# Optimization experiments

Hardware: AMD Instinct MI355X
Metric: run time of the kernel (lower is better)

The kernel has to match this reference:

```python
import jax, jax.numpy as jnp
import numpy as np

B, T, M = 4, 1024, 512
H, K, V = 8, 64, 64
EPS = 1e-6


def setup_inputs() -> dict:
    key = jax.random.key(0)
    ks = jax.random.split(key, 8)
    s = 1.0 / np.sqrt(M)
    return {
        "query": jax.random.normal(ks[0], (B, T, M), jnp.float32),
        "key": jax.random.normal(ks[1], (B, T, M), jnp.float32),
        "value": jax.random.normal(ks[2], (B, T, M), jnp.float32),
        "Wq": jax.random.normal(ks[3], (M, H * K), jnp.float32) * s,
        "Wk": jax.random.normal(ks[4], (M, H * K), jnp.float32) * s,
        "Wv": jax.random.normal(ks[5], (M, H * V), jnp.float32) * s,
        # gate linear is zero-initialized in the original (Constant(0.0)); use
        # small random weights so the gate path is exercised numerically.
        "Wg": jax.random.normal(ks[6], (M, H * V), jnp.float32) * (0.02 * s),
        "bg": jnp.zeros((H * V,), jnp.float32),
        "Wo": jax.random.normal(ks[7], (H * V, M), jnp.float32) * (1.0 / np.sqrt(H * V)),
    }


def _phi(x):
    return jax.nn.elu(x) + 1.0


def reference(query, key, value, Wq, Wk, Wv, Wg, bg, Wo):
    # projections -> [B, T, H, d]
    q = (query @ Wq).reshape(B, T, H, K)
    k = (key @ Wk).reshape(B, T, H, K)
    v = (value @ Wv).reshape(B, T, H, V)

    qf = _phi(q)
    kf = _phi(k)

    # multiplicative value gate from the raw value input
    gate = jax.nn.sigmoid((value @ Wg + bg).reshape(B, T, H, V))
    v = v * (2.0 * gate)

    # visualization attention map: qf . kf, causal, row-normalized
    scores = jnp.einsum("bthk,bshk->bhts", qf, kf)  # [B,H,T,T]
    causal = (jnp.arange(T)[None, :] <= jnp.arange(T)[:, None]).astype(scores.dtype)
    scores = scores * causal[None, None]
    att_map = scores / (jnp.sum(scores, axis=-1, keepdims=True) + EPS)

    # causal linear attention via cumulative sums (Tq == Tk so the idx-take
    # in the original is an identity gather)
    kv = jnp.einsum("bthk,bthv->bthkv", kf, v)  # [B,T,H,K,V]
    kv_cum = jnp.cumsum(kv, axis=1)
    k_cum = jnp.cumsum(kf, axis=1)               # [B,T,H,K]

    numer = jnp.einsum("bthk,bthkv->bthv", qf, kv_cum)
    denom = jnp.einsum("bthk,bthk->bth", qf, k_cum) + EPS
    out = (numer / denom[..., None]).reshape(B, T, H * V)
    out = out @ Wo  # [B,T,M]
    return out, att_map
```

## Files before the change

### kernel.cpp

```cpp
#include <hip/hip_runtime.h>
#include <cstdint>

#define TDIM 1024
#define BDIM 4
#define EPSF 1e-6f

#define OFF_KSUM  32768u
#define OFF_KV    65536u
#define FLOAT_BYTES 8650752u
#define UOFF_QP 0u
#define UOFF_KP 2097152u
#define UOFF_VP 4194304u
#define UOFF_NB 6291456u
#define UOFF_WQ 8388608u
#define UOFF_WK 8650752u
#define UOFF_WV 8912896u
#define UOFF_WG 9175040u
#define UOFF_WO 9437184u

typedef short bf16x8 __attribute__((ext_vector_type(8)));
typedef float f32x4  __attribute__((ext_vector_type(4)));
typedef unsigned short ushort_t;

union bfu { int4 i4; unsigned short us[8]; bf16x8 v; };

__device__ __forceinline__ float phi_f(float x)  { return x > 0.f ? x + 1.f : __expf(x); }
__device__ __forceinline__ float sigm_f(float x) { return 1.f / (1.f + __expf(-x)); }
__device__ __forceinline__ unsigned short f2b(float x) {
    union { float f; unsigned u; } v; v.f = x;
    return (unsigned short)((v.u + 0x7FFFu + ((v.u >> 16) & 1u)) >> 16);
}
__device__ __forceinline__ float b2f(unsigned short s) {
    union { unsigned u; float f; } v; v.u = (unsigned)s << 16; return v.f;
}
__device__ __forceinline__ int4 pack8(float4 a, float4 b) {
    bfu u;
    u.us[0] = f2b(a.x); u.us[1] = f2b(a.y); u.us[2] = f2b(a.z); u.us[3] = f2b(a.w);
    u.us[4] = f2b(b.x); u.us[5] = f2b(b.y); u.us[6] = f2b(b.z); u.us[7] = f2b(b.w);
    return u.i4;
}
#define FMA4(ACC, S, V) do { (ACC).x += (S)*(V).x; (ACC).y += (S)*(V).y; \
                             (ACC).z += (S)*(V).z; (ACC).w += (S)*(V).w; } while (0)

__global__ __launch_bounds__(256) void castwt_all(const float* __restrict__ W0,
                                                  const float* __restrict__ W1,
                                                  const float* __restrict__ W2,
                                                  const float* __restrict__ W3,
                                                  const float* __restrict__ W4,
                                                  ushort_t* __restrict__ T0,
                                                  ushort_t* __restrict__ T1,
                                                  ushort_t* __restrict__ T2,
                                                  ushort_t* __restrict__ T3,
                                                  ushort_t* __restrict__ T4) {
    const float* W; ushort_t* Wt;
    switch (blockIdx.z) {
        case 0: W = W0; Wt = T0; break;
        case 1: W = W1; Wt = T1; break;
        case 2: W = W2; Wt = T2; break;
        case 3: W = W3; Wt = T3; break;
        default: W = W4; Wt = T4; break;
    }
    __shared__ unsigned short tile[32][36];
    const int t = threadIdx.x;
    const int r0 = blockIdx.y * 32, c0 = blockIdx.x * 32;
    {
        const int r = t >> 3, c4 = (t & 7) * 4;
        float4 x = *(const float4*)(W + (size_t)(r0 + r) * 512 + c0 + c4);
        tile[c4 + 0][r] = f2b(x.x); tile[c4 + 1][r] = f2b(x.y);
        tile[c4 + 2][r] = f2b(x.z); tile[c4 + 3][r] = f2b(x.w);
    }
    __syncthreads();
    const int c = t >> 3, r4 = (t & 7) * 4;
    ushort4 o;
    o.x = tile[c][r4 + 0]; o.y = tile[c][r4 + 1];
    o.z = tile[c][r4 + 2]; o.w = tile[c][r4 + 3];
    *(ushort4*)(Wt + (size_t)(c0 + c) * 512 + r0 + r4) = o;
}

__global__ __launch_bounds__(256) void proj_k(const float* __restrict__ query,
                                              const float* __restrict__ key_,
                                              const float* __restrict__ value,
                                              const ushort_t* __restrict__ wqt,
                                              const ushort_t* __restrict__ wkt,
                                              const ushort_t* __restrict__ wvt,
                                              const ushort_t* __restrict__ wgt,
                                              const float* __restrict__ bg,
                                              ushort_t* __restrict__ qp,
                                              ushort_t* __restrict__ kp,
                                              ushort_t* __restrict__ vp) {
    __shared__ __align__(16) unsigned short As[2][4096];
    __shared__ __align__(16) unsigned short Bs[2][4096];
    __shared__ __align__(16) unsigned short Bs2[2][4096];
    const int z = blockIdx.z;
    const float* A = (z == 0) ? query : (z == 1) ? key_ : value;
    const ushort_t* B0 = (z == 0) ? wqt : (z == 1) ? wkt : wvt;
    ushort_t* outp = (z == 0) ? qp : (z == 1) ? kp : vp;
    const bool dual = (z == 2);

    const int tid = threadIdx.x;
    const int row0 = blockIdx.x * 64, n0 = blockIdx.y * 64;
    const int w = tid >> 6, lane = tid & 63;
    const int cc = tid & 7, rr = tid >> 3;
    const int fm = lane & 15, fq = lane >> 4;
    const int la0 = (cc * 64 + (rr ^ cc)) * 8;
    const int la1 = (cc * 64 + ((rr + 32) ^ cc)) * 8;

    f32x4 acc[4], acc2[4];
#pragma unroll
    for (int i = 0; i < 4; i++) {
        acc[i]  = (f32x4){0.f, 0.f, 0.f, 0.f};
        acc2[i] = (f32x4){0.f, 0.f, 0.f, 0.f};
    }

    const float*   aptr = A  + (size_t)(row0 + rr) * 512 + cc * 8;
    const ushort_t* bptr = B0 + (size_t)(n0 + rr) * 512 + cc * 8;
    const ushort_t* gptr = wgt + (size_t)(n0 + rr) * 512 + cc * 8;

    float4 a0 = *(const float4*)(aptr);
    float4 a1 = *(const float4*)(aptr + 4);
    float4 a2 = *(const float4*)(aptr + 32 * 512);
    float4 a3 = *(const float4*)(aptr + 32 * 512 + 4);
    int4 b0 = *(const int4*)(bptr);
    int4 b1 = *(const int4*)(bptr + 32 * 512);
    int4 g0 = {0, 0, 0, 0}, g1 = {0, 0, 0, 0};
    if (dual) { g0 = *(const int4*)(gptr); g1 = *(const int4*)(gptr + 32 * 512); }
    *(int4*)&As[0][la0] = pack8(a0, a1);
    *(int4*)&As[0][la1] = pack8(a2, a3);
    *(int4*)&Bs[0][la0] = b0; *(int4*)&Bs[0][la1] = b1;
    if (dual) { *(int4*)&Bs2[0][la0] = g0; *(int4*)&Bs2[0][la1] = g1; }
    __syncthreads();

    for (int kti = 0; kti < 8; kti++) {
        const int buf = kti & 1;
        if (kti < 7) {
            const int off = (kti + 1) * 64;
            a0 = *(const float4*)(aptr + off);
            a1 = *(const float4*)(aptr + off + 4);
            a2 = *(const float4*)(aptr + off + 32 * 512);
            a3 = *(const float4*)(aptr + off + 32 * 512 + 4);
            b0 = *(const int4*)(bptr + off);
            b1 = *(const int4*)(bptr + off + 32 * 512);
            if (dual) {
                g0 = *(const int4*)(gptr + off);
                g1 = *(const int4*)(gptr + off + 32 * 512);
            }
        }
        if (dual) {
#pragma unroll
            for (int j = 0; j < 2; j++) {
                const int cu = j * 4 + fq;
                bf16x8 af = *(const bf16x8*)&As[buf][(cu * 64 + ((w * 16 + fm) ^ cu)) * 8];
#pragma unroll
                for (int nb = 0; nb < 4; nb++) {
                    bf16x8 bv = *(const bf16x8*)&Bs[buf][(cu * 64 + ((nb * 16 + fm) ^ cu)) * 8];
                    bf16x8 gv = *(const bf16x8*)&Bs2[buf][(cu * 64 + ((nb * 16 + fm) ^ cu)) * 8];
                    acc[nb]  = __builtin_amdgcn_mfma_f32_16x16x32_bf16(af, bv, acc[nb], 0, 0, 0);
                    acc2[nb] = __builtin_amdgcn_mfma_f32_16x16x32_bf16(af, gv, acc2[nb], 0, 0, 0);
                }
            }
        } else {
#pragma unroll
            for (int j = 0; j < 2; j++) {
                const int cu = j * 4 + fq;
                bf16x8 af = *(const bf16x8*)&As[buf][(cu * 64 + ((w * 16 + fm) ^ cu)) * 8];
#pragma unroll
                for (int nb = 0; nb < 4; nb++) {
                    bf16x8 bv = *(const bf16x8*)&Bs[buf][(cu * 64 + ((nb * 16 + fm) ^ cu)) * 8];
                    acc[nb] = __builtin_amdgcn_mfma_f32_16x16x32_bf16(af, bv, acc[nb], 0, 0, 0);
                }
            }
        }
        if (kti < 7) {
            const int nb_ = buf ^ 1;
            *(int4*)&As[nb_][la0] = pack8(a0, a1);
            *(int4*)&As[nb_][la1] = pack8(a2, a3);
            *(int4*)&Bs[nb_][la0] = b0; *(int4*)&Bs[nb_][la1] = b1;
            if (dual) { *(int4*)&Bs2[nb_][la0] = g0; *(int4*)&Bs2[nb_][la1] = g1; }
            __syncthreads();
        }
    }

#pragma unroll
    for (int nb = 0; nb < 4; nb++) {
        const int col = n0 + nb * 16 + fm;
        const float bb = dual ? bg[col] : 0.f;
#pragma unroll
        for (int r = 0; r < 4; r++) {
            const int row = row0 + w * 16 + fq * 4 + r;
            const float v = acc[nb][r];
            const ushort_t o = dual ? f2b(v * 2.f * sigm_f(acc2[nb][r] + bb))
                                    : f2b(phi_f(v));
            outp[(size_t)row * 512 + col] = o;
        }
    }
}

__global__ __launch_bounds__(256) void outproj_k(const ushort_t* __restrict__ A,
                                                 const ushort_t* __restrict__ Bt,
                                                 float* __restrict__ out) {
    __shared__ __align__(16) unsigned short As[2][4096];
    __shared__ __align__(16) unsigned short Bs[2][4096];
    const int tid = threadIdx.x;
    const int row0 = blockIdx.x * 64, n0 = blockIdx.y * 64;
    const int w = tid >> 6, lane = tid & 63;
    const int cc = tid & 7, rr = tid >> 3;
    const int fm = lane & 15, fq = lane >> 4;
    const int la0 = (cc * 64 + (rr ^ cc)) * 8;
    const int la1 = (cc * 64 + ((rr + 32) ^ cc)) * 8;

    f32x4 acc[4];
#pragma unroll
    for (int i = 0; i < 4; i++) acc[i] = (f32x4){0.f, 0.f, 0.f, 0.f};

    const ushort_t* aptr = A  + (size_t)(row0 + rr) * 512 + cc * 8;
    const ushort_t* bptr = Bt + (size_t)(n0 + rr) * 512 + cc * 8;
    int4 ra0 = *(const int4*)(aptr);
    int4 ra1 = *(const int4*)(aptr + 32 * 512);
    int4 rb0 = *(const int4*)(bptr);
    int4 rb1 = *(const int4*)(bptr + 32 * 512);
    *(int4*)&As[0][la0] = ra0; *(int4*)&As[0][la1] = ra1;
    *(int4*)&Bs[0][la0] = rb0; *(int4*)&Bs[0][la1] = rb1;
    __syncthreads();

    for (int kti = 0; kti < 8; kti++) {
        const int buf = kti & 1;
        if (kti < 7) {
            const int off = (kti + 1) * 64;
            ra0 = *(const int4*)(aptr + off);
            ra1 = *(const int4*)(aptr + off + 32 * 512);
            rb0 = *(const int4*)(bptr + off);
            rb1 = *(const int4*)(bptr + off + 32 * 512);
        }
#pragma unroll
        for (int j = 0; j < 2; j++) {
            const int cu = j * 4 + fq;
            bf16x8 af = *(const bf16x8*)&As[buf][(cu * 64 + ((w * 16 + fm) ^ cu)) * 8];
#pragma unroll
            for (int nb = 0; nb < 4; nb++) {
                bf16x8 bv = *(const bf16x8*)&Bs[buf][(cu * 64 + ((nb * 16 + fm) ^ cu)) * 8];
                acc[nb] = __builtin_amdgcn_mfma_f32_16x16x32_bf16(af, bv, acc[nb], 0, 0, 0);
            }
        }
        if (kti < 7) {
            const int nb_ = buf ^ 1;
            *(int4*)&As[nb_][la0] = ra0; *(int4*)&As[nb_][la1] = ra1;
            *(int4*)&Bs[nb_][la0] = rb0; *(int4*)&Bs[nb_][la1] = rb1;
            __syncthreads();
        }
    }
#pragma unroll
    for (int nb = 0; nb < 4; nb++) {
        const int col = n0 + nb * 16 + fm;
#pragma unroll
        for (int r = 0; r < 4; r++) {
            const int row = row0 + w * 16 + fq * 4 + r;
            __builtin_nontemporal_store(acc[nb][r], &out[(size_t)row * 512 + col]);
        }
    }
}

__global__ __launch_bounds__(256) void chunksum_k(const ushort_t* __restrict__ kb,
                                                  const ushort_t* __restrict__ vb,
                                                  float* __restrict__ kv,
                                                  float* __restrict__ ksum) {
    __shared__ __align__(16) float kf_c[64][68];
    __shared__ __align__(16) float vg_c[64][68];
    const int tid = threadIdx.x;
    const int bh = blockIdx.x, c = blockIdx.y;
    const int b = bh >> 3, h = bh & 7;
    const int r = tid >> 2, qq = tid & 3;
    {
        const size_t rowbase = ((size_t)(b * TDIM + c * 64 + r)) * 512 + h * 64 + qq * 16;
        bfu k0, k1, v0, v1;
        k0.i4 = *(const int4*)(kb + rowbase);
        k1.i4 = *(const int4*)(kb + rowbase + 8);
        v0.i4 = *(const int4*)(vb + rowbase);
        v1.i4 = *(const int4*)(vb + rowbase + 8);
#pragma unroll
        for (int j = 0; j < 8; j++) {
            kf_c[r][qq * 16 + j]     = b2f(k0.us[j]);
            kf_c[r][qq * 16 + 8 + j] = b2f(k1.us[j]);
            vg_c[r][qq * 16 + j]     = b2f(v0.us[j]);
            vg_c[r][qq * 16 + 8 + j] = b2f(v1.us[j]);
        }
    }
    __syncthreads();
    const int k0i = (tid >> 4) * 4;
    const int v0i = (tid & 15) * 4;
    float4 a4[4];
#pragma unroll
    for (int i = 0; i < 4; i++) a4[i] = make_float4(0.f, 0.f, 0.f, 0.f);
    for (int t = 0; t < 64; t++) {
        float4 kk4 = *(const float4*)&kf_c[t][k0i];
        float4 vv  = *(const float4*)&vg_c[t][v0i];
        FMA4(a4[0], kk4.x, vv); FMA4(a4[1], kk4.y, vv);
        FMA4(a4[2], kk4.z, vv); FMA4(a4[3], kk4.w, vv);
    }
    const size_t base = (size_t)(bh * 16 + c) * 64;
#pragma unroll
    for (int i = 0; i < 4; i++)
        *(float4*)(kv + (base + k0i + i) * 64 + v0i) = a4[i];
    if (tid < 64) {
        float s = 0.f;
        for (int t = 0; t < 64; t++) s += kf_c[t][tid];
        ksum[base + tid] = s;
    }
}

__global__ __launch_bounds__(256) void fused_k(const ushort_t* __restrict__ qb,
                                               const ushort_t* __restrict__ kb,
                                               const ushort_t* __restrict__ vb,
                                               const float* __restrict__ kvc,
                                               const float* __restrict__ ksum,
                                               ushort_t* __restrict__ nbo,
                                               float* __restrict__ att) {
    extern __shared__ __align__(16) char smem[];
    unsigned short* qs   = (unsigned short*)smem;
    unsigned short* ksb  = qs + 4096;
    unsigned short* vrow = ksb + 8192;
    float* kvf  = (float*)(vrow + 64 * 72);
    float* sc   = kvf + 64 * 68;
    float* kpre = sc + 64 * 68;
    float* ps   = kpre + 64;
    float* inv_s = ps + 256;

    const int tid = threadIdx.x;
    const int bh = blockIdx.x, diag = 15 - (int)blockIdx.y;
    const int tt0 = diag * 64;
    const int b = bh >> 3, h = bh & 7;
    const int w = tid >> 6, lane = tid & 63;
    const int fm = lane & 15, fq = lane >> 4;
    const int rr = tid >> 3, cc = tid & 7;
    const int la0 = (cc * 64 + (rr ^ cc)) * 8;
    const int la1 = (cc * 64 + ((rr + 32) ^ cc)) * 8;

    const ushort_t* kbase = kb + ((size_t)(b * TDIM + rr)) * 512 + h * 64 + cc * 8;

    {
        const ushort_t* qptr = qb + ((size_t)(b * TDIM + tt0 + rr)) * 512 + h * 64 + cc * 8;
        *(int4*)&qs[la0] = *(const int4*)qptr;
        *(int4*)&qs[la1] = *(const int4*)(qptr + 32 * 512);
        const ushort_t* kptr = kbase + (size_t)tt0 * 512;
        *(int4*)&ksb[la0] = *(const int4*)kptr;
        *(int4*)&ksb[la1] = *(const int4*)(kptr + 32 * 512);
        const int r = tid >> 2, qq = tid & 3;
        const ushort_t* vptr = vb + ((size_t)(b * TDIM + tt0 + r)) * 512 + h * 64 + qq * 16;
        *(int4*)&vrow[r * 72 + qq * 16]     = *(const int4*)vptr;
        *(int4*)&vrow[r * 72 + qq * 16 + 8] = *(const int4*)(vptr + 8);
        float4 a4[4];
#pragma unroll
        for (int u = 0; u < 4; u++) a4[u] = make_float4(0.f, 0.f, 0.f, 0.f);
        for (int c2 = 0; c2 < diag; c2++) {
            const float* p = kvc + (size_t)(bh * 16 + c2) * 4096 + r * 64 + qq * 16;
#pragma unroll
            for (int u = 0; u < 4; u++) {
                float4 x = *(const float4*)(p + 4 * u);
                a4[u].x += x.x; a4[u].y += x.y; a4[u].z += x.z; a4[u].w += x.w;
            }
        }
#pragma unroll
        for (int u = 0; u < 4; u++) *(float4*)&kvf[r * 68 + qq * 16 + 4 * u] = a4[u];
        if (tid < 64) {
            float s = 0.f;
            for (int c2 = 0; c2 < diag; c2++)
                s += ksum[(size_t)(bh * 16 + c2) * 64 + tid];
            kpre[tid] = s;
        }
    }
    __syncthreads();

    f32x4 sa[4];
    {
        int4 rk0 = {0,0,0,0}, rk1 = {0,0,0,0};
        if (diag > 0) {
            rk0 = *(const int4*)(kbase);
            rk1 = *(const int4*)(kbase + 32 * 512);
        }
#pragma unroll
        for (int i = 0; i < 4; i++) sa[i] = (f32x4){0.f, 0.f, 0.f, 0.f};
#pragma unroll
        for (int j = 0; j < 2; j++) {
            const int cu = j * 4 + fq;
            bf16x8 aqf = *(const bf16x8*)&qs[(cu * 64 + ((w * 16 + fm) ^ cu)) * 8];
#pragma unroll
            for (int nb = 0; nb < 4; nb++) {
                bf16x8 bk = *(const bf16x8*)&ksb[(cu * 64 + ((nb * 16 + fm) ^ cu)) * 8];
                sa[nb] = __builtin_amdgcn_mfma_f32_16x16x32_bf16(aqf, bk, sa[nb], 0, 0, 0);
            }
        }
#pragma unroll
        for (int nb = 0; nb < 4; nb++) {
            const int s_l = nb * 16 + fm;
#pragma unroll
            for (int r = 0; r < 4; r++) {
                const int t_l = w * 16 + fq * 4 + r;
                sc[t_l * 68 + s_l] = (s_l <= t_l) ? sa[nb][r] : 0.f;
            }
        }
        if (diag > 0) {
            *(int4*)&ksb[4096 + la0] = rk0;
            *(int4*)&ksb[4096 + la1] = rk1;
        }
    }
    __syncthreads();

    {
        const int rw = tid >> 2, sq = tid & 3;
        float p = 0.f;
#pragma unroll
        for (int s = sq * 16; s < sq * 16 + 16; s++) p += sc[rw * 68 + s];
#pragma unroll
        for (int kd = sq * 16; kd < sq * 16 + 16; kd++) {
            const int cu = kd >> 3;
            p += b2f(qs[(cu * 64 + (rw ^ cu)) * 8 + (kd & 7)]) * kpre[kd];
        }
        ps[rw * 4 + sq] = p;
    }
    __syncthreads();
    {
        const int rw = tid >> 2, sq = tid & 3;
        if (sq == 0) {
            float den = ps[rw * 4] + ps[rw * 4 + 1] + ps[rw * 4 + 2] + ps[rw * 4 + 3];
            inv_s[rw] = 1.f / (den + EPSF);
        }
    }
    __syncthreads();

    {
        f32x4 oa[4];
#pragma unroll
        for (int i = 0; i < 4; i++) oa[i] = (f32x4){0.f, 0.f, 0.f, 0.f};
        bf16x8 aqv[2], apv[2];
#pragma unroll
        for (int j = 0; j < 2; j++) {
            const int cu = j * 4 + fq;
            aqv[j] = *(const bf16x8*)&qs[(cu * 64 + ((w * 16 + fm) ^ cu)) * 8];
            bfu t;
#pragma unroll
            for (int e2 = 0; e2 < 8; e2++) t.us[e2] = f2b(sc[(w * 16 + fm) * 68 + cu * 8 + e2]);
            apv[j] = t.v;
        }
#pragma unroll
        for (int nb = 0; nb < 4; nb++) {
            const int v = nb * 16 + fm;
#pragma unroll
            for (int j = 0; j < 2; j++) {
                const int cu = j * 4 + fq;
                bfu tkv, tv;
#pragma unroll
                for (int e = 0; e < 8; e++) {
                    tkv.us[e] = f2b(kvf[(cu * 8 + e) * 68 + v]);
                    tv.us[e]  = vrow[(cu * 8 + e) * 72 + v];
                }
                oa[nb] = __builtin_amdgcn_mfma_f32_16x16x32_bf16(aqv[j], tkv.v, oa[nb], 0, 0, 0);
                oa[nb] = __builtin_amdgcn_mfma_f32_16x16x32_bf16(apv[j], tv.v, oa[nb], 0, 0, 0);
            }
        }
#pragma unroll
        for (int nb = 0; nb < 4; nb++) {
            const int vcol = nb * 16 + fm;
#pragma unroll
            for (int r = 0; r < 4; r++) {
                const int t_l = w * 16 + fq * 4 + r;
                const float val = oa[nb][r] * inv_s[t_l];
                nbo[((size_t)(b * TDIM + tt0 + t_l)) * 512 + h * 64 + vcol] = f2b(val);
            }
        }
    }

    bf16x8 aq[2];
    float invr[4];
#pragma unroll
    for (int j = 0; j < 2; j++) {
        const int cu = j * 4 + fq;
        aq[j] = *(const bf16x8*)&qs[(cu * 64 + ((w * 16 + fm) ^ cu)) * 8];
    }
#pragma unroll
    for (int r = 0; r < 4; r++) invr[r] = inv_s[w * 16 + fq * 4 + r];

    float* attb = att + (size_t)bh * TDIM * TDIM;
    int4 rk0, rk1;
    for (int st = 0; st < diag; st++) {
        const int bsel = (st + 1) & 1;
        if (st + 1 < diag) {
            const size_t off = (size_t)(st + 1) * 64 * 512;
            rk0 = *(const int4*)(kbase + off);
            rk1 = *(const int4*)(kbase + off + 32 * 512);
        }
        f32x4 pa[4];
#pragma unroll
        for (int i = 0; i < 4; i++) pa[i] = (f32x4){0.f, 0.f, 0.f, 0.f};
#pragma unroll
        for (int j = 0; j < 2; j++) {
            const int cu = j * 4 + fq;
#pragma unroll
            for (int nb = 0; nb < 4; nb++) {
                bf16x8 bk = *(const bf16x8*)&ksb[bsel * 4096 +
                                                 (cu * 64 + ((nb * 16 + fm) ^ cu)) * 8];
                pa[nb] = __builtin_amdgcn_mfma_f32_16x16x32_bf16(aq[j], bk, pa[nb], 0, 0, 0);
            }
        }
        const int s0 = st * 64;
#pragma unroll
        for (int nb = 0; nb < 4; nb++) {
            const int s_g = s0 + nb * 16 + fm;
#pragma unroll
            for (int r = 0; r < 4; r++) {
                const int t_g = tt0 + w * 16 + fq * 4 + r;
                __builtin_nontemporal_store(pa[nb][r] * invr[r],
                                            &attb[(size_t)t_g * TDIM + s_g]);
            }
        }
        if (st + 1 < diag) {
            *(int4*)&ksb[(bsel ^ 1) * 4096 + la0] = rk0;
            *(int4*)&ksb[(bsel ^ 1) * 4096 + la1] = rk1;
            __syncthreads();
        }
    }
#pragma unroll
    for (int nb = 0; nb < 4; nb++) {
        const int s_l = nb * 16 + fm;
#pragma unroll
        for (int r = 0; r < 4; r++) {
            const int t_l = w * 16 + fq * 4 + r;
            const float val = (s_l <= t_l) ? sa[nb][r] * invr[r] : 0.f;
            __builtin_nontemporal_store(val,
                &attb[(size_t)(tt0 + t_l) * TDIM + tt0 + s_l]);
        }
    }
    {
        const f32x4 z = (f32x4){0.f, 0.f, 0.f, 0.f};
        const int r = tid >> 2, qq = tid & 3;
        float* rowp = attb + (size_t)(tt0 + r) * TDIM;
        for (int c0 = (diag + 1) * 64 + qq * 4; c0 < TDIM; c0 += 16)
            __builtin_nontemporal_store(z, (f32x4*)(rowp + c0));
    }
}

extern "C" void kernel_launch(void* const* d_in, const int* in_sizes, int n_in,
                              void* d_out, int out_size, void* d_ws, size_t ws_size,
                              hipStream_t stream) {
    (void)in_sizes; (void)n_in; (void)out_size; (void)ws_size;
    const float* query = (const float*)d_in[0];
    const float* key   = (const float*)d_in[1];
    const float* value = (const float*)d_in[2];
    const float* Wq    = (const float*)d_in[3];
    const float* Wk    = (const float*)d_in[4];
    const float* Wv    = (const float*)d_in[5];
    const float* Wg    = (const float*)d_in[6];
    const float* bg    = (const float*)d_in[7];
    const float* Wo    = (const float*)d_in[8];
    float* out = (float*)d_out;
    float* att = (float*)d_out + 2097152;
    float* ws  = (float*)d_ws;
    float* ksum = ws + OFF_KSUM;
    float* kv   = ws + OFF_KV;
    ushort_t* ub  = (ushort_t*)((char*)d_ws + FLOAT_BYTES);
    ushort_t* qp  = ub + UOFF_QP;
    ushort_t* kp  = ub + UOFF_KP;
    ushort_t* vp  = ub + UOFF_VP;
    ushort_t* nbp = ub + UOFF_NB;
    ushort_t* wqt = ub + UOFF_WQ;
    ushort_t* wkt = ub + UOFF_WK;
    ushort_t* wvt = ub + UOFF_WV;
    ushort_t* wgt = ub + UOFF_WG;
    ushort_t* wot = ub + UOFF_WO;

    dim3 blk(256);
    castwt_all<<<dim3(16, 16, 5), blk, 0, stream>>>(Wq, Wk, Wv, Wg, Wo,
                                                    wqt, wkt, wvt, wgt, wot);
    proj_k<<<dim3(64, 8, 3), blk, 0, stream>>>(query, key, value,
                                               wqt, wkt, wvt, wgt, bg, qp, kp, vp);
    chunksum_k<<<dim3(32, 16), blk, 0, stream>>>(kp, vp, kv, ksum);
    fused_k<<<dim3(32, 16), blk, 70144, stream>>>(qp, kp, vp, kv, ksum, nbp, att);
    outproj_k<<<dim3(64, 8), blk, 0, stream>>>(nbp, wot, out);
}
```

Baseline: 244.4 us.

## Split attention-map writes into separate per-tile kernel with stored inverse denominators

The attention-map generation is moved out of fused_k into a new attmap_k kernel launched over (bh, query tile, key tile), with fused_k writing the per-row inverse denominators to workspace. Before, each fused_k block looped serially over all earlier key tiles and zero-filled its row tail, so work was unbalanced across diagonals. The aim is to spread the 128 MB att-map writes over many more independent blocks for better bandwidth use and load balance. In exchange it adds a kernel launch, reloads Q and K tiles per block, and keeps fused_k's LDS within static limits.

```diff
diff --git a/kernel.cpp b/kernel.cpp
--- a/kernel.cpp
+++ b/kernel.cpp
@@ -5,6 +5,7 @@
 #define BDIM 4
 #define EPSF 1e-6f
 
+#define OFF_INV   0u
 #define OFF_KSUM  32768u
 #define OFF_KV    65536u
 #define FLOAT_BYTES 8650752u
@@ -313,16 +314,15 @@
                                                const float* __restrict__ kvc,
                                                const float* __restrict__ ksum,
                                                ushort_t* __restrict__ nbo,
-                                               float* __restrict__ att) {
-    extern __shared__ __align__(16) char smem[];
-    unsigned short* qs   = (unsigned short*)smem;
-    unsigned short* ksb  = qs + 4096;
-    unsigned short* vrow = ksb + 8192;
-    float* kvf  = (float*)(vrow + 64 * 72);
-    float* sc   = kvf + 64 * 68;
-    float* kpre = sc + 64 * 68;
-    float* ps   = kpre + 64;
-    float* inv_s = ps + 256;
+                                               float* __restrict__ invw) {
+    __shared__ __align__(16) unsigned short qs[4096];
+    __shared__ __align__(16) unsigned short ksb[4096];
+    __shared__ __align__(16) unsigned short vrow[64 * 72];
+    __shared__ __align__(16) float kvf[64 * 68];
+    __shared__ __align__(16) float sc[64 * 68];
+    __shared__ float kpre[64];
+    __shared__ float ps[256];
+    __shared__ float inv_s[64];
 
     const int tid = threadIdx.x;
     const int bh = blockIdx.x, diag = 15 - (int)blockIdx.y;
@@ -334,13 +334,11 @@
     const int la0 = (cc * 64 + (rr ^ cc)) * 8;
     const int la1 = (cc * 64 + ((rr + 32) ^ cc)) * 8;
 
-    const ushort_t* kbase = kb + ((size_t)(b * TDIM + rr)) * 512 + h * 64 + cc * 8;
-
     {
         const ushort_t* qptr = qb + ((size_t)(b * TDIM + tt0 + rr)) * 512 + h * 64 + cc * 8;
         *(int4*)&qs[la0] = *(const int4*)qptr;
         *(int4*)&qs[la1] = *(const int4*)(qptr + 32 * 512);
-        const ushort_t* kptr = kbase + (size_t)tt0 * 512;
+        const ushort_t* kptr = kb + ((size_t)(b * TDIM + tt0 + rr)) * 512 + h * 64 + cc * 8;
         *(int4*)&ksb[la0] = *(const int4*)kptr;
         *(int4*)&ksb[la1] = *(const int4*)(kptr + 32 * 512);
         const int r = tid >> 2, qq = tid & 3;
@@ -369,13 +367,8 @@
     }
     __syncthreads();
 
-    f32x4 sa[4];
-    {
-        int4 rk0 = {0,0,0,0}, rk1 = {0,0,0,0};
-        if (diag > 0) {
-            rk0 = *(const int4*)(kbase);
-            rk1 = *(const int4*)(kbase + 32 * 512);
-        }
+    {
+        f32x4 sa[4];
 #pragma unroll
         for (int i = 0; i < 4; i++) sa[i] = (f32x4){0.f, 0.f, 0.f, 0.f};
 #pragma unroll
@@ -397,10 +390,6 @@
                 sc[t_l * 68 + s_l] = (s_l <= t_l) ? sa[nb][r] : 0.f;
             }
         }
-        if (diag > 0) {
-            *(int4*)&ksb[4096 + la0] = rk0;
-            *(int4*)&ksb[4096 + la1] = rk1;
-        }
     }
     __syncthreads();
 
@@ -421,7 +410,9 @@
         const int rw = tid >> 2, sq = tid & 3;
         if (sq == 0) {
             float den = ps[rw * 4] + ps[rw * 4 + 1] + ps[rw * 4 + 2] + ps[rw * 4 + 3];
-            inv_s[rw] = 1.f / (den + EPSF);
+            const float iv = 1.f / (den + EPSF);
+            inv_s[rw] = iv;
+            invw[(size_t)(bh * 16 + diag) * 64 + rw] = iv;
         }
     }
     __syncthreads();
@@ -467,73 +458,72 @@
             }
         }
     }
-
-    bf16x8 aq[2];
-    float invr[4];
+}
+
+__global__ __launch_bounds__(256) void attmap_k(const ushort_t* __restrict__ qb,
+                                                const ushort_t* __restrict__ kb,
+                                                const float* __restrict__ invw,
+                                                float* __restrict__ att) {
+    const int tid = threadIdx.x;
+    const int bh = blockIdx.x, tt = blockIdx.y, st = blockIdx.z;
+    float* attb = att + ((size_t)bh * TDIM + (size_t)tt * 64) * TDIM + (size_t)st * 64;
+
+    if (st > tt) {
+        const int r = tid >> 2, c0 = (tid & 3) * 4;
+        const f32x4 z = (f32x4){0.f, 0.f, 0.f, 0.f};
+        float* rp = attb + (size_t)r * TDIM + c0;
+#pragma unroll
+        for (int i = 0; i < 4; i++)
+            __builtin_nontemporal_store(z, (f32x4*)(rp + 16 * i));
+        return;
+    }
+
+    __shared__ __align__(16) unsigned short qs[4096];
+    __shared__ __align__(16) unsigned short ks[4096];
+    __shared__ float inv_l[64];
+    const int b = bh >> 3, h = bh & 7;
+    const int rr = tid >> 3, cc = tid & 7;
+    const int la0 = (cc * 64 + (rr ^ cc)) * 8;
+    const int la1 = (cc * 64 + ((rr + 32) ^ cc)) * 8;
+
+    const ushort_t* qptr = qb + ((size_t)(b * TDIM + tt * 64 + rr)) * 512 + h * 64 + cc * 8;
+    *(int4*)&qs[la0] = *(const int4*)qptr;
+    *(int4*)&qs[la1] = *(const int4*)(qptr + 32 * 512);
+    const ushort_t* kptr = kb + ((size_t)(b * TDIM + st * 64 + rr)) * 512 + h * 64 + cc * 8;
+    *(int4*)&ks[la0] = *(const int4*)kptr;
+    *(int4*)&ks[la1] = *(const int4*)(kptr + 32 * 512);
+    if (tid < 64) inv_l[tid] = invw[(size_t)(bh * 16 + tt) * 64 + tid];
+    __syncthreads();
+
+    const int w = tid >> 6, lane = tid & 63;
+    const int fm = lane & 15, fq = lane >> 4;
+    f32x4 pa[4];
+#pragma unroll
+    for (int i = 0; i < 4; i++) pa[i] = (f32x4){0.f, 0.f, 0.f, 0.f};
 #pragma unroll
     for (int j = 0; j < 2; j++) {
         const int cu = j * 4 + fq;
-        aq[j] = *(const bf16x8*)&qs[(cu * 64 + ((w * 16 + fm) ^ cu)) * 8];
-    }
-#pragma unroll
-    for (int r = 0; r < 4; r++) invr[r] = inv_s[w * 16 + fq * 4 + r];
-
-    float* attb = att + (size_t)bh * TDIM * TDIM;
-    int4 rk0, rk1;
-    for (int st = 0; st < diag; st++) {
-        const int bsel = (st + 1) & 1;
-        if (st + 1 < diag) {
-            const size_t off = (size_t)(st + 1) * 64 * 512;
-            rk0 = *(const int4*)(kbase + off);
-            rk1 = *(const int4*)(kbase + off + 32 * 512);
-        }
-        f32x4 pa[4];
-#pragma unroll
-        for (int i = 0; i < 4; i++) pa[i] = (f32x4){0.f, 0.f, 0.f, 0.f};
-#pragma unroll
-        for (int j = 0; j < 2; j++) {
-            const int cu = j * 4 + fq;
-#pragma unroll
-            for (int nb = 0; nb < 4; nb++) {
-                bf16x8 bk = *(const bf16x8*)&ksb[bsel * 4096 +
-                                                 (cu * 64 + ((nb * 16 + fm) ^ cu)) * 8];
-                pa[nb] = __builtin_amdgcn_mfma_f32_16x16x32_bf16(aq[j], bk, pa[nb], 0, 0, 0);
-            }
-        }
-        const int s0 = st * 64;
+        bf16x8 aq = *(const bf16x8*)&qs[(cu * 64 + ((w * 16 + fm) ^ cu)) * 8];
 #pragma unroll
         for (int nb = 0; nb < 4; nb++) {
-            const int s_g = s0 + nb * 16 + fm;
-#pragma unroll
-            for (int r = 0; r < 4; r++) {
-                const int t_g = tt0 + w * 16 + fq * 4 + r;
-                __builtin_nontemporal_store(pa[nb][r] * invr[r],
-                                            &attb[(size_t)t_g * TDIM + s_g]);
-            }
-        }
-        if (st + 1 < diag) {
-            *(int4*)&ksb[(bsel ^ 1) * 4096 + la0] = rk0;
-            *(int4*)&ksb[(bsel ^ 1) * 4096 + la1] = rk1;
-            __syncthreads();
-        }
-    }
+            bf16x8 bk = *(const bf16x8*)&ks[(cu * 64 + ((nb * 16 + fm) ^ cu)) * 8];
+            pa[nb] = __builtin_amdgcn_mfma_f32_16x16x32_bf16(aq, bk, pa[nb], 0, 0, 0);
+        }
+    }
+    float invr[4];
+#pragma unroll
+    for (int r = 0; r < 4; r++) invr[r] = inv_l[w * 16 + fq * 4 + r];
+    const bool dg = (st == tt);
 #pragma unroll
     for (int nb = 0; nb < 4; nb++) {
         const int s_l = nb * 16 + fm;
 #pragma unroll
         for (int r = 0; r < 4; r++) {
             const int t_l = w * 16 + fq * 4 + r;
-            const float val = (s_l <= t_l) ? sa[nb][r] * invr[r] : 0.f;
-            __builtin_nontemporal_store(val,
-                &attb[(size_t)(tt0 + t_l) * TDIM + tt0 + s_l]);
-        }
-    }
-    {
-        const f32x4 z = (f32x4){0.f, 0.f, 0.f, 0.f};
-        const int r = tid >> 2, qq = tid & 3;
-        float* rowp = attb + (size_t)(tt0 + r) * TDIM;
-        for (int c0 = (diag + 1) * 64 + qq * 4; c0 < TDIM; c0 += 16)
-            __builtin_nontemporal_store(z, (f32x4*)(rowp + c0));
+            float val = pa[nb][r] * invr[r];
+            if (dg && s_l > t_l) val = 0.f;
+            __builtin_nontemporal_store(val, &attb[(size_t)t_l * TDIM + s_l]);
+        }
     }
 }
 
@@ -553,6 +543,7 @@
     float* out = (float*)d_out;
     float* att = (float*)d_out + 2097152;
     float* ws  = (float*)d_ws;
+    float* invw = ws + OFF_INV;
     float* ksum = ws + OFF_KSUM;
     float* kv   = ws + OFF_KV;
     ushort_t* ub  = (ushort_t*)((char*)d_ws + FLOAT_BYTES);
@@ -572,6 +563,7 @@
     proj_k<<<dim3(64, 8, 3), blk, 0, stream>>>(query, key, value,
                                                wqt, wkt, wvt, wgt, bg, qp, kp, vp);
     chunksum_k<<<dim3(32, 16), blk, 0, stream>>>(kp, vp, kv, ksum);
-    fused_k<<<dim3(32, 16), blk, 70144, stream>>>(qp, kp, vp, kv, ksum, nbp, att);
+    fused_k<<<dim3(32, 16), blk, 0, stream>>>(qp, kp, vp, kv, ksum, nbp, invw);
+    attmap_k<<<dim3(32, 16, 16), blk, 0, stream>>>(qp, kp, invw, att);
     outproj_k<<<dim3(64, 8), blk, 0, stream>>>(nbp, wot, out);
 }
```

Result: slower. 259.3 us (+6.1%).
